# Optimization experiments

Hardware: AMD Instinct MI355X
Metric: run time of the kernel (lower is better)

The kernel has to match this reference:

```python
import jax, jax.numpy as jnp
import numpy as np

N1 = 50000; N2 = 50000; F = 256; HID = 64; H = 8; DH = HID // H; L = 2; E = 800000


def setup_inputs() -> dict:
    key = jax.random.key(0)
    ks = jax.random.split(key, 20)
    f32 = jnp.float32
    rn = lambda k, shape, s=0.1: jax.random.normal(k, shape, dtype=f32) * s
    inp = {}
    inp['x1'] = jax.random.normal(ks[0], (N1, F), dtype=f32)
    inp['x2'] = jax.random.normal(ks[1], (N2, F), dtype=f32)
    # row 0 = source node ids, row 1 = destination node ids
    inp['edge12'] = jax.random.randint(ks[2], (2, E), 0, N2)  # n1 -> n2
    inp['edge21'] = jax.random.randint(ks[3], (2, E), 0, N1)  # n2 -> n1
    inp['w_in'] = rn(ks[4], (2, HID, F))
    inp['b_in'] = rn(ks[5], (2, HID))
    inp['kw'] = rn(ks[6], (L, 2, HID, HID)); inp['kb'] = rn(ks[7], (L, 2, HID))
    inp['qw'] = rn(ks[8], (L, 2, HID, HID)); inp['qb'] = rn(ks[9], (L, 2, HID))
    inp['vw'] = rn(ks[10], (L, 2, HID, HID)); inp['vb'] = rn(ks[11], (L, 2, HID))
    inp['aw'] = rn(ks[12], (L, 2, HID, HID)); inp['ab'] = rn(ks[13], (L, 2, HID))
    inp['skip'] = jax.random.normal(ks[14], (L, 2), dtype=f32)
    inp['a_rel'] = rn(ks[15], (L, 2, H, DH, DH), 0.3)
    inp['m_rel'] = rn(ks[16], (L, 2, H, DH, DH), 0.3)
    inp['p_rel'] = jnp.ones((L, 2, H), dtype=f32)
    return inp


def _segment_softmax(logits, seg, n):
    # logits: [E, H], seg: [E] destination ids
    m = jax.ops.segment_max(logits, seg, num_segments=n)
    e = jnp.exp(logits - m[seg])
    s = jax.ops.segment_sum(e, seg, num_segments=n)
    return e / s[seg]


def reference(x1, x2, edge12, edge21, w_in, b_in, kw, kb, qw, qb, vw, vb, aw, ab,
              skip, a_rel, m_rel, p_rel):
    scale = jnp.asarray(1.0 / np.sqrt(DH), x1.dtype)

    def kqv(h, l, t):
        k = (h @ kw[l, t].T + kb[l, t]).reshape(-1, H, DH)
        q = (h @ qw[l, t].T + qb[l, t]).reshape(-1, H, DH)
        v = (h @ vw[l, t].T + vb[l, t]).reshape(-1, H, DH)
        return k, q, v

    def message(k_src, v_src, q_dst, edge, ar, mr, pr, n_dst):
        kr = jnp.einsum('nhd,hde->nhe', k_src, ar)   # per-node relation projection
        vr = jnp.einsum('nhd,hde->nhe', v_src, mr)
        s, d = edge[0], edge[1]
        logit = jnp.einsum('ehd,ehd->eh', q_dst[d], kr[s]) * pr[None, :] * scale
        alpha = _segment_softmax(logit, d, n_dst)     # [E, H]
        out = jax.ops.segment_sum(alpha[:, :, None] * vr[s], d, num_segments=n_dst)
        return out.reshape(n_dst, HID)

    def update(o, h, l, t):
        o = jax.nn.gelu(o, approximate=False) @ aw[l, t].T + ab[l, t]
        beta = jax.nn.sigmoid(skip[l, t])
        return beta * o + (1.0 - beta) * h

    # per-node-type input Linear + ReLU stem
    h1 = jax.nn.relu(x1 @ w_in[0].T + b_in[0])
    h2 = jax.nn.relu(x2 @ w_in[1].T + b_in[1])

    outs1, outs2 = [], []
    for l in range(L):
        k1, q1, v1 = kqv(h1, l, 0)
        k2, q2, v2 = kqv(h2, l, 1)
        o2 = message(k1, v1, q2, edge12, a_rel[l, 0], m_rel[l, 0], p_rel[l, 0], h2.shape[0])
        o1 = message(k2, v2, q1, edge21, a_rel[l, 1], m_rel[l, 1], p_rel[l, 1], h1.shape[0])
        h1 = update(o1, h1, l, 0)
        h2 = update(o2, h2, l, 1)
        outs1.append(h1)
        outs2.append(h2)

    Em = jnp.concatenate(outs1, axis=1)  # [N1, HID*L]
    Ed = jnp.concatenate(outs2, axis=1)  # [N2, HID*L]
    return Em, Ed
```

## Files before the change

kernel.cpp:

```cpp
#include <hip/hip_runtime.h>
#include <hip/hip_bf16.h>
#include <math.h>

typedef __attribute__((ext_vector_type(8))) short bf16x8;
typedef __attribute__((ext_vector_type(4))) float f32x4;
typedef __attribute__((ext_vector_type(4))) unsigned int u32x4;
typedef __attribute__((ext_vector_type(4))) int i32x4;
typedef unsigned short ushort_t;

#define BUCKET_SHIFT 6
#define BUCKET_CAP   64

__device__ inline short f2b(float f) {
    __hip_bfloat16 h = __float2bfloat16(f);
    return __builtin_bit_cast(short, h);
}
__device__ inline float b2f(unsigned short u) {
    return __builtin_bit_cast(float, (unsigned int)u << 16);
}
__device__ inline float blo(unsigned int w) {
    return __builtin_bit_cast(float, w << 16);
}
__device__ inline float bhi(unsigned int w) {
    return __builtin_bit_cast(float, w & 0xffff0000u);
}

__global__ __launch_bounds__(256) void prep_kernel(
    const float* __restrict__ w_in,
    const float* __restrict__ kw, const float* __restrict__ kb,
    const float* __restrict__ qw, const float* __restrict__ qb,
    const float* __restrict__ vw, const float* __restrict__ vb,
    const float* __restrict__ aw,
    const float* __restrict__ a_rel, const float* __restrict__ m_rel,
    const float* __restrict__ p_rel,
    short* __restrict__ wstem, short* __restrict__ Wcat,
    float* __restrict__ Bcat, short* __restrict__ Awb)
{
    int bid = blockIdx.x, tid = threadIdx.x;
    if (bid >= 4) {
        int t = bid - 4;
        for (int i = tid; i < 16384; i += 256)
            wstem[t * 16384 + i] = f2b(w_in[t * 16384 + i]);
        return;
    }
    int base = bid;
    const float* KW = kw + base * 4096;
    const float* QW = qw + base * 4096;
    const float* VW = vw + base * 4096;
    const float* AR = a_rel + base * 512;
    const float* MR = m_rel + base * 512;
    const float* PR = p_rel + base * 8;
    short* WC = Wcat + base * 12288;
    float* BC = Bcat + base * 192;

    for (int i = tid; i < 4096; i += 256) WC[i] = f2b(QW[i]);
    for (int i = tid; i < 4096; i += 256) {
        int out = i >> 6, in = i & 63;
        int h = out >> 3, e = out & 7;
        float s = PR[h] * 0.35355339059327373f;
        float acc = 0.f;
        #pragma unroll
        for (int d = 0; d < 8; ++d) acc += KW[(h * 8 + d) * 64 + in] * AR[h * 64 + d * 8 + e];
        WC[4096 + i] = f2b(acc * s);
    }
    for (int i = tid; i < 4096; i += 256) {
        int out = i >> 6, in = i & 63;
        int h = out >> 3, e = out & 7;
        float acc = 0.f;
        #pragma unroll
        for (int d = 0; d < 8; ++d) acc += VW[(h * 8 + d) * 64 + in] * MR[h * 64 + d * 8 + e];
        WC[8192 + i] = f2b(acc);
    }
    if (tid < 64) {
        BC[tid] = qb[base * 64 + tid];
    } else if (tid < 128) {
        int out = tid - 64;
        int h = out >> 3, e = out & 7;
        float s = PR[h] * 0.35355339059327373f;
        float acc = 0.f;
        #pragma unroll
        for (int d = 0; d < 8; ++d) acc += kb[base * 64 + h * 8 + d] * AR[h * 64 + d * 8 + e];
        BC[64 + out] = acc * s;
    } else if (tid < 192) {
        int out = tid - 128;
        int h = out >> 3, e = out & 7;
        float acc = 0.f;
        #pragma unroll
        for (int d = 0; d < 8; ++d) acc += vb[base * 64 + h * 8 + d] * MR[h * 64 + d * 8 + e];
        BC[128 + out] = acc;
    }
    for (int i = tid; i < 4096; i += 256) Awb[base * 4096 + i] = f2b(aw[base * 4096 + i]);
}

__global__ __launch_bounds__(256) void stem2_mfma(
    const float* __restrict__ X1, const float* __restrict__ X2,
    const short* __restrict__ Wb, const float* __restrict__ B1, const float* __restrict__ B2,
    short* __restrict__ H1, short* __restrict__ H2, int N1, int N2, int nt1)
{
    const float* X; const short* Wsrc; const float* B; short* Hb; int N; int tb;
    if (blockIdx.x < nt1) { X = X1; Wsrc = Wb;         B = B1; Hb = H1; N = N1; tb = blockIdx.x; }
    else                  { X = X2; Wsrc = Wb + 16384; B = B2; Hb = H2; N = N2; tb = blockIdx.x - nt1; }
    __shared__ short Ws[64 * 256];
    int tid = threadIdx.x;
    #pragma unroll
    for (int k = 0; k < 8; ++k) {
        int u = tid + k * 256;
        int row = u >> 5, c = u & 31;
        u32x4 v = *reinterpret_cast<const u32x4*>(Wsrc + row * 256 + c * 8);
        *reinterpret_cast<u32x4*>(&Ws[row * 256 + ((c ^ (row & 7)) << 3)]) = v;
    }
    __syncthreads();
    int w = tid >> 6, l = tid & 63;
    int g = l >> 4, q = l & 15;
    int row = tb * 64 + w * 16 + q;
    bool rok = row < N;
    f32x4 acc[4] = {};
    const float* xr = X + (size_t)row * 256 + g * 8;
    #pragma unroll
    for (int s = 0; s < 8; ++s) {
        bf16x8 a = {};
        if (rok) {
            float4 x0 = *reinterpret_cast<const float4*>(xr + s * 32);
            float4 x1 = *reinterpret_cast<const float4*>(xr + s * 32 + 4);
            a[0] = f2b(x0.x); a[1] = f2b(x0.y); a[2] = f2b(x0.z); a[3] = f2b(x0.w);
            a[4] = f2b(x1.x); a[5] = f2b(x1.y); a[6] = f2b(x1.z); a[7] = f2b(x1.w);
        }
        #pragma unroll
        for (int n = 0; n < 4; ++n) {
            int br = n * 16 + q;
            int c = s * 4 + g;
            bf16x8 b = *reinterpret_cast<bf16x8*>(&Ws[br * 256 + ((c ^ (br & 7)) << 3)]);
            acc[n] = __builtin_amdgcn_mfma_f32_16x16x32_bf16(a, b, acc[n], 0, 0, 0);
        }
    }
    int orow0 = tb * 64 + w * 16 + g * 4;
    #pragma unroll
    for (int n = 0; n < 4; ++n) {
        int col = n * 16 + q;
        float bias = B[col];
        #pragma unroll
        for (int r = 0; r < 4; ++r) {
            int orow = orow0 + r;
            if (orow < N)
                Hb[(size_t)orow * 64 + col] = f2b(fmaxf(acc[n][r] + bias, 0.f));
        }
    }
}

__global__ __launch_bounds__(256) void kqv2_mfma(
    const short* __restrict__ H1, const short* __restrict__ Wc1, const float* __restrict__ Bc1,
    short* __restrict__ Q1, short* __restrict__ KV1, int N1,
    const short* __restrict__ H2, const short* __restrict__ Wc2, const float* __restrict__ Bc2,
    short* __restrict__ Q2, short* __restrict__ KV2, int N2, int nt1)
{
    const short* Hb; const short* Wcat; const float* Bcat; short* Qb; short* KV; int N; int tb;
    if (blockIdx.x < nt1) { Hb = H1; Wcat = Wc1; Bcat = Bc1; Qb = Q1; KV = KV1; N = N1; tb = blockIdx.x; }
    else                  { Hb = H2; Wcat = Wc2; Bcat = Bc2; Qb = Q2; KV = KV2; N = N2; tb = blockIdx.x - nt1; }
    __shared__ short Ws[192 * 64];
    int tid = threadIdx.x;
    #pragma unroll
    for (int k = 0; k < 6; ++k) {
        int u = tid + k * 256;
        int row = u >> 3, c = u & 7;
        u32x4 v = *reinterpret_cast<const u32x4*>(Wcat + row * 64 + c * 8);
        *reinterpret_cast<u32x4*>(&Ws[row * 64 + ((c ^ (row & 7)) << 3)]) = v;
    }
    __syncthreads();
    int w = tid >> 6, l = tid & 63;
    int g = l >> 4, q = l & 15;
    int arow = tb * 64 + w * 16 + q;
    bool rok = arow < N;
    bf16x8 a0 = {}, a1 = {};
    if (rok) {
        a0 = *reinterpret_cast<const bf16x8*>(Hb + (size_t)arow * 64 + g * 8);
        a1 = *reinterpret_cast<const bf16x8*>(Hb + (size_t)arow * 64 + 32 + g * 8);
    }
    f32x4 acc[12] = {};
    #pragma unroll
    for (int n = 0; n < 12; ++n) {
        int br = n * 16 + q;
        bf16x8 b0 = *reinterpret_cast<bf16x8*>(&Ws[br * 64 + ((0 * 4 + g) ^ (br & 7)) * 8]);
        acc[n] = __builtin_amdgcn_mfma_f32_16x16x32_bf16(a0, b0, acc[n], 0, 0, 0);
        bf16x8 b1 = *reinterpret_cast<bf16x8*>(&Ws[br * 64 + ((1 * 4 + g) ^ (br & 7)) * 8]);
        acc[n] = __builtin_amdgcn_mfma_f32_16x16x32_bf16(a1, b1, acc[n], 0, 0, 0);
    }
    int orow0 = tb * 64 + w * 16 + g * 4;
    #pragma unroll
    for (int n = 0; n < 12; ++n) {
        int col = n * 16 + q;
        float bias = Bcat[col];
        #pragma unroll
        for (int r = 0; r < 4; ++r) {
            int orow = orow0 + r;
            if (orow < N) {
                float v = acc[n][r] + bias;
                if (n < 4)      Qb[(size_t)orow * 64 + col]                 = f2b(v);
                else if (n < 8) KV[(size_t)orow * 128 + 2 * (col - 64)]     = f2b(v);
                else            KV[(size_t)orow * 128 + 2 * (col - 128) + 1] = f2b(v);
            }
        }
    }
}

__global__ __launch_bounds__(256) void bucket8v_kernel(
    const int* __restrict__ srcA, const int* __restrict__ dstA,
    const int* __restrict__ srcB, const int* __restrict__ dstB,
    int* __restrict__ cntA, int* __restrict__ cntB,
    ushort_t* __restrict__ csA, ushort_t* __restrict__ csB,
    int E, int rangeA, int rangeB, int G)
{
    int grp = blockIdx.x & 7;
    int blk = blockIdx.x >> 3;
    int loA = grp * rangeA, hiA = loA + rangeA;
    int loB = grp * rangeB, hiB = loB + rangeB;
    int stride = G * 256;
    int E4 = E >> 2;
    for (int v = blk * 256 + threadIdx.x; v < 2 * E4; v += stride) {
        if (v < E4) {
            i32x4 d4 = __builtin_nontemporal_load(reinterpret_cast<const i32x4*>(dstA) + v);
            int base = v * 4;
            if (d4.x >= loA && d4.x < hiA) { int p = atomicAdd(&cntA[d4.x], 1); if (p < BUCKET_CAP) csA[((size_t)d4.x << BUCKET_SHIFT) + p] = (ushort_t)srcA[base]; }
            if (d4.y >= loA && d4.y < hiA) { int p = atomicAdd(&cntA[d4.y], 1); if (p < BUCKET_CAP) csA[((size_t)d4.y << BUCKET_SHIFT) + p] = (ushort_t)srcA[base + 1]; }
            if (d4.z >= loA && d4.z < hiA) { int p = atomicAdd(&cntA[d4.z], 1); if (p < BUCKET_CAP) csA[((size_t)d4.z << BUCKET_SHIFT) + p] = (ushort_t)srcA[base + 2]; }
            if (d4.w >= loA && d4.w < hiA) { int p = atomicAdd(&cntA[d4.w], 1); if (p < BUCKET_CAP) csA[((size_t)d4.w << BUCKET_SHIFT) + p] = (ushort_t)srcA[base + 3]; }
        } else {
            int vv = v - E4;
            i32x4 d4 = __builtin_nontemporal_load(reinterpret_cast<const i32x4*>(dstB) + vv);
            int base = vv * 4;
            if (d4.x >= loB && d4.x < hiB) { int p = atomicAdd(&cntB[d4.x], 1); if (p < BUCKET_CAP) csB[((size_t)d4.x << BUCKET_SHIFT) + p] = (ushort_t)srcB[base]; }
            if (d4.y >= loB && d4.y < hiB) { int p = atomicAdd(&cntB[d4.y], 1); if (p < BUCKET_CAP) csB[((size_t)d4.y << BUCKET_SHIFT) + p] = (ushort_t)srcB[base + 1]; }
            if (d4.z >= loB && d4.z < hiB) { int p = atomicAdd(&cntB[d4.z], 1); if (p < BUCKET_CAP) csB[((size_t)d4.z << BUCKET_SHIFT) + p] = (ushort_t)srcB[base + 2]; }
            if (d4.w >= loB && d4.w < hiB) { int p = atomicAdd(&cntB[d4.w], 1); if (p < BUCKET_CAP) csB[((size_t)d4.w << BUCKET_SHIFT) + p] = (ushort_t)srcB[base + 3]; }
        }
    }
    int tail = E & 3;
    if (blk == 0 && threadIdx.x < 2 * tail) {
        int t = threadIdx.x;
        if (t < tail) {
            int i = E - tail + t;
            int d = dstA[i];
            if (d >= loA && d < hiA) { int p = atomicAdd(&cntA[d], 1); if (p < BUCKET_CAP) csA[((size_t)d << BUCKET_SHIFT) + p] = (ushort_t)srcA[i]; }
        } else {
            int i = E - tail + (t - tail);
            int d = dstB[i];
            if (d >= loB && d < hiB) { int p = atomicAdd(&cntB[d], 1); if (p < BUCKET_CAP) csB[((size_t)d << BUCKET_SHIFT) + p] = (ushort_t)srcB[i]; }
        }
    }
}

__global__ __launch_bounds__(256) void gather8_kernel(
    const int* __restrict__ cntA, const ushort_t* __restrict__ csA,
    const short* __restrict__ QA, const short* __restrict__ KVA, short* __restrict__ GA, int NA,
    const int* __restrict__ cntB, const ushort_t* __restrict__ csB,
    const short* __restrict__ QB, const short* __restrict__ KVB, short* __restrict__ GB, int NB)
{
    int grp = blockIdx.x & 7;
    int localBlock = (blockIdx.x >> 3) * 4 + (grp & 3);
    const int* cnt; const ushort_t* cs; const short* Qb; const short* KV; short* G; int N;
    if (grp < 4) { cnt = cntA; cs = csA; Qb = QA; KV = KVA; G = GA; N = NA; }
    else         { cnt = cntB; cs = csB; Qb = QB; KV = KVB; G = GB; N = NB; }
    int d = localBlock * 4 + (threadIdx.x >> 6);
    if (d >= N) return;
    int lane = threadIdx.x & 63;
    int j = lane & 15;
    int sub = lane >> 4;
    int deg = min(cnt[d], BUCKET_CAP);
    uint2 qw = *reinterpret_cast<const uint2*>(Qb + (size_t)d * 64 + 4 * j);
    float q0 = blo(qw.x), q1 = bhi(qw.x), q2 = blo(qw.y), q3 = bhi(qw.y);
    float a0 = 0.f, a1 = 0.f, a2 = 0.f, a3 = 0.f, den = 0.f;
    int idv = (lane < deg) ? (int)cs[((size_t)d << BUCKET_SHIFT) + lane] : 0;
    for (int i = 0; i < deg; i += 4) {
        int idx = i + sub;
        bool valid = idx < deg;
        int s = __shfl(idv, valid ? idx : 0);
        u32x4 w = *reinterpret_cast<const u32x4*>(KV + (size_t)s * 128 + 8 * j);
        float t = q0 * blo(w.x);
        t = fmaf(q1, blo(w.y), t);
        t = fmaf(q2, blo(w.z), t);
        t = fmaf(q3, blo(w.w), t);
        t += __shfl_xor(t, 1);
        float e = valid ? __expf(t) : 0.f;
        den += e;
        a0 = fmaf(e, bhi(w.x), a0);
        a1 = fmaf(e, bhi(w.y), a1);
        a2 = fmaf(e, bhi(w.z), a2);
        a3 = fmaf(e, bhi(w.w), a3);
    }
    a0 += __shfl_xor(a0, 16); a1 += __shfl_xor(a1, 16);
    a2 += __shfl_xor(a2, 16); a3 += __shfl_xor(a3, 16);
    den += __shfl_xor(den, 16);
    a0 += __shfl_xor(a0, 32); a1 += __shfl_xor(a1, 32);
    a2 += __shfl_xor(a2, 32); a3 += __shfl_xor(a3, 32);
    den += __shfl_xor(den, 32);
    if (lane < 16) {
        float r = (den > 0.f) ? 1.f / den : 0.f;
        float o0 = a0 * r, o1 = a1 * r, o2 = a2 * r, o3 = a3 * r;
        float g0 = 0.5f * o0 * (1.f + erff(o0 * 0.70710678118654752f));
        float g1 = 0.5f * o1 * (1.f + erff(o1 * 0.70710678118654752f));
        float g2 = 0.5f * o2 * (1.f + erff(o2 * 0.70710678118654752f));
        float g3 = 0.5f * o3 * (1.f + erff(o3 * 0.70710678118654752f));
        uint2 pw;
        pw.x = ((unsigned int)(unsigned short)f2b(g0)) | (((unsigned int)(unsigned short)f2b(g1)) << 16);
        pw.y = ((unsigned int)(unsigned short)f2b(g2)) | (((unsigned int)(unsigned short)f2b(g3)) << 16);
        *reinterpret_cast<uint2*>(G + (size_t)d * 64 + 4 * j) = pw;
    }
}

__global__ __launch_bounds__(256) void updkqv_mfma(
    const short* __restrict__ G1, const short* __restrict__ Aw1, const float* __restrict__ Ab1,
    const float* __restrict__ sk1, short* __restrict__ H1, float* __restrict__ Out1, int N1,
    const short* __restrict__ G2, const short* __restrict__ Aw2, const float* __restrict__ Ab2,
    const float* __restrict__ sk2, short* __restrict__ H2, float* __restrict__ Out2, int N2,
    const short* __restrict__ Wc1n, const float* __restrict__ Bc1n,
    short* __restrict__ Q1, short* __restrict__ KV1,
    const short* __restrict__ Wc2n, const float* __restrict__ Bc2n,
    short* __restrict__ Q2, short* __restrict__ KV2,
    int nt1, int outColOff)
{
    const short* G; const short* Awb; const float* Ab; const float* skipp;
    short* Hb; float* Out; int N; int tb;
    const short* Wcat; const float* Bcat; short* Qb; short* KV;
    if (blockIdx.x < nt1) {
        G = G1; Awb = Aw1; Ab = Ab1; skipp = sk1; Hb = H1; Out = Out1; N = N1; tb = blockIdx.x;
        Wcat = Wc1n; Bcat = Bc1n; Qb = Q1; KV = KV1;
    } else {
        G = G2; Awb = Aw2; Ab = Ab2; skipp = sk2; Hb = H2; Out = Out2; N = N2; tb = blockIdx.x - nt1;
        Wcat = Wc2n; Bcat = Bc2n; Qb = Q2; KV = KV2;
    }
    __shared__ short Ws[192 * 64];
    __shared__ short hs[64][64];
    int tid = threadIdx.x;
    #pragma unroll
    for (int k = 0; k < 6; ++k) {
        int u = tid + k * 256;
        int row = u >> 3, c = u & 7;
        u32x4 v = *reinterpret_cast<const u32x4*>(Wcat + row * 64 + c * 8);
        *reinterpret_cast<u32x4*>(&Ws[row * 64 + ((c ^ (row & 7)) << 3)]) = v;
    }
    int w = tid >> 6, l = tid & 63;
    int g = l >> 4, q = l & 15;
    bf16x8 bfw[4][2];
    #pragma unroll
    for (int n = 0; n < 4; ++n)
        #pragma unroll
        for (int s = 0; s < 2; ++s)
            bfw[n][s] = *reinterpret_cast<const bf16x8*>(Awb + (n * 16 + q) * 64 + s * 32 + g * 8);
    float beta = 1.f / (1.f + __expf(-skipp[0]));
    int arow = tb * 64 + w * 16 + q;
    bool rok = arow < N;
    bf16x8 ua0 = {}, ua1 = {};
    if (rok) {
        ua0 = *reinterpret_cast<const bf16x8*>(G + (size_t)arow * 64 + g * 8);
        ua1 = *reinterpret_cast<const bf16x8*>(G + (size_t)arow * 64 + 32 + g * 8);
    }
    f32x4 uacc[4] = {};
    #pragma unroll
    for (int n = 0; n < 4; ++n) {
        uacc[n] = __builtin_amdgcn_mfma_f32_16x16x32_bf16(ua0, bfw[n][0], uacc[n], 0, 0, 0);
        uacc[n] = __builtin_amdgcn_mfma_f32_16x16x32_bf16(ua1, bfw[n][1], uacc[n], 0, 0, 0);
    }
    int orow0 = tb * 64 + w * 16 + g * 4;
    int lrow0 = w * 16 + g * 4;
    #pragma unroll
    for (int n = 0; n < 4; ++n) {
        int col = n * 16 + q;
        float bias = Ab[col];
        #pragma unroll
        for (int r = 0; r < 4; ++r) {
            int orow = orow0 + r;
            if (orow < N) {
                float hold = b2f(((const unsigned short*)Hb)[(size_t)orow * 64 + col]);
                float hnew = beta * (uacc[n][r] + bias) + (1.f - beta) * hold;
                short hb16 = f2b(hnew);
                Out[(size_t)orow * 128 + outColOff + col] = hnew;
                Hb[(size_t)orow * 64 + col] = hb16;
                hs[lrow0 + r][col] = hb16;
            } else {
                hs[lrow0 + r][col] = 0;
            }
        }
    }
    __syncthreads();
    bf16x8 a0 = *reinterpret_cast<const bf16x8*>(&hs[w * 16 + q][g * 8]);
    bf16x8 a1 = *reinterpret_cast<const bf16x8*>(&hs[w * 16 + q][32 + g * 8]);
    f32x4 acc[12] = {};
    #pragma unroll
    for (int n = 0; n < 12; ++n) {
        int br = n * 16 + q;
        bf16x8 b0 = *reinterpret_cast<bf16x8*>(&Ws[br * 64 + ((0 * 4 + g) ^ (br & 7)) * 8]);
        acc[n] = __builtin_amdgcn_mfma_f32_16x16x32_bf16(a0, b0, acc[n], 0, 0, 0);
        bf16x8 b1 = *reinterpret_cast<bf16x8*>(&Ws[br * 64 + ((1 * 4 + g) ^ (br & 7)) * 8]);
        acc[n] = __builtin_amdgcn_mfma_f32_16x16x32_bf16(a1, b1, acc[n], 0, 0, 0);
    }
    #pragma unroll
    for (int n = 0; n < 12; ++n) {
        int col = n * 16 + q;
        float bias = Bcat[col];
        #pragma unroll
        for (int r = 0; r < 4; ++r) {
            int orow = orow0 + r;
            if (orow < N) {
                float v = acc[n][r] + bias;
                if (n < 4)      Qb[(size_t)orow * 64 + col]                  = f2b(v);
                else if (n < 8) KV[(size_t)orow * 128 + 2 * (col - 64)]      = f2b(v);
                else            KV[(size_t)orow * 128 + 2 * (col - 128) + 1] = f2b(v);
            }
        }
    }
}

__global__ __launch_bounds__(256) void update2_mfma(
    const short* __restrict__ G1, const short* __restrict__ Aw1, const float* __restrict__ Ab1,
    const float* __restrict__ sk1, short* __restrict__ H1, float* __restrict__ Out1, int N1,
    const short* __restrict__ G2, const short* __restrict__ Aw2, const float* __restrict__ Ab2,
    const float* __restrict__ sk2, short* __restrict__ H2, float* __restrict__ Out2, int N2,
    int nt1, int outColOff)
{
    const short* G; const short* Awb; const float* Ab; const float* skipp;
    short* Hb; float* Out; int N; int tb;
    if (blockIdx.x < nt1) { G = G1; Awb = Aw1; Ab = Ab1; skipp = sk1; Hb = H1; Out = Out1; N = N1; tb = blockIdx.x; }
    else                  { G = G2; Awb = Aw2; Ab = Ab2; skipp = sk2; Hb = H2; Out = Out2; N = N2; tb = blockIdx.x - nt1; }
    int tid = threadIdx.x;
    int w = tid >> 6, l = tid & 63;
    int g = l >> 4, q = l & 15;
    bf16x8 bf[4][2];
    #pragma unroll
    for (int n = 0; n < 4; ++n)
        #pragma unroll
        for (int s = 0; s < 2; ++s)
            bf[n][s] = *reinterpret_cast<const bf16x8*>(Awb + (n * 16 + q) * 64 + s * 32 + g * 8);
    float beta = 1.f / (1.f + __expf(-skipp[0]));
    int arow = tb * 64 + w * 16 + q;
    bool rok = arow < N;
    bf16x8 a0 = {}, a1 = {};
    if (rok) {
        a0 = *reinterpret_cast<const bf16x8*>(G + (size_t)arow * 64 + g * 8);
        a1 = *reinterpret_cast<const bf16x8*>(G + (size_t)arow * 64 + 32 + g * 8);
    }
    f32x4 acc[4] = {};
    #pragma unroll
    for (int n = 0; n < 4; ++n) {
        acc[n] = __builtin_amdgcn_mfma_f32_16x16x32_bf16(a0, bf[n][0], acc[n], 0, 0, 0);
        acc[n] = __builtin_amdgcn_mfma_f32_16x16x32_bf16(a1, bf[n][1], acc[n], 0, 0, 0);
    }
    int orow0 = tb * 64 + w * 16 + g * 4;
    #pragma unroll
    for (int n = 0; n < 4; ++n) {
        int col = n * 16 + q;
        float bias = Ab[col];
        #pragma unroll
        for (int r = 0; r < 4; ++r) {
            int orow = orow0 + r;
            if (orow < N) {
                float hold = b2f(((const unsigned short*)Hb)[(size_t)orow * 64 + col]);
                float hnew = beta * (acc[n][r] + bias) + (1.f - beta) * hold;
                Out[(size_t)orow * 128 + outColOff + col] = hnew;
                Hb[(size_t)orow * 64 + col] = f2b(hnew);
            }
        }
    }
}

extern "C" void kernel_launch(void* const* d_in, const int* in_sizes, int n_in,
                              void* d_out, int out_size, void* d_ws, size_t ws_size,
                              hipStream_t stream) {
    const float* x1    = (const float*)d_in[0];
    const float* x2    = (const float*)d_in[1];
    const int*   e12   = (const int*)d_in[2];
    const int*   e21   = (const int*)d_in[3];
    const float* w_in  = (const float*)d_in[4];
    const float* b_in  = (const float*)d_in[5];
    const float* kw    = (const float*)d_in[6];
    const float* kb    = (const float*)d_in[7];
    const float* qw    = (const float*)d_in[8];
    const float* qb    = (const float*)d_in[9];
    const float* vw    = (const float*)d_in[10];
    const float* vb    = (const float*)d_in[11];
    const float* aw    = (const float*)d_in[12];
    const float* ab    = (const float*)d_in[13];
    const float* skip  = (const float*)d_in[14];
    const float* a_rel = (const float*)d_in[15];
    const float* m_rel = (const float*)d_in[16];
    const float* p_rel = (const float*)d_in[17];

    int N1 = in_sizes[0] / 256;
    int N2 = in_sizes[1] / 256;
    int E  = in_sizes[2] / 2;

    float* out = (float*)d_out;

    char* wsp = (char*)d_ws;
    auto alloc = [&](size_t bytes) { void* p = wsp; wsp += (bytes + 255) & ~(size_t)255; return p; };
    short* hb1   = (short*)alloc((size_t)N1 * 64 * 2);
    short* hb2   = (short*)alloc((size_t)N2 * 64 * 2);
    short* qb1   = (short*)alloc((size_t)N1 * 64 * 2);
    short* qb2   = (short*)alloc((size_t)N2 * 64 * 2);
    short* kv1   = (short*)alloc((size_t)N1 * 128 * 2);
    short* kv2   = (short*)alloc((size_t)N2 * 128 * 2);
    short* g1    = (short*)alloc((size_t)N1 * 64 * 2);
    short* g2    = (short*)alloc((size_t)N2 * 64 * 2);
    short* wstem = (short*)alloc(2 * 16384 * 2);
    short* WcatB = (short*)alloc(4 * 12288 * 2);
    float* BcatB = (float*)alloc(4 * 192 * 4);
    short* AwbB  = (short*)alloc(4 * 4096 * 2);
    int* cnts    = (int*)alloc((size_t)(N1 + N2) * 4);
    int* cnt12   = cnts;
    int* cnt21   = cnts + N2;
    ushort_t* csr12 = (ushort_t*)alloc(((size_t)N2 << BUCKET_SHIFT) * 2);
    ushort_t* csr21 = (ushort_t*)alloc(((size_t)N1 << BUCKET_SHIFT) * 2);

    const int BLK = 256;
    int nt1 = (N1 + 63) / 64;
    int nt2 = (N2 + 63) / 64;

    int rangeA = (N2 + 7) / 8;
    int rangeB = (N1 + 7) / 8;
    const int G8 = 512;

    prep_kernel<<<6, BLK, 0, stream>>>(w_in, kw, kb, qw, qb, vw, vb, aw,
                                       a_rel, m_rel, p_rel, wstem, WcatB, BcatB, AwbB);

    hipMemsetAsync(cnts, 0, (size_t)(N1 + N2) * 4, stream);
    bucket8v_kernel<<<8 * G8, BLK, 0, stream>>>(e12, e12 + E, e21, e21 + E,
                                                cnt12, cnt21, csr12, csr21,
                                                E, rangeA, rangeB, G8);

    stem2_mfma<<<nt1 + nt2, BLK, 0, stream>>>(x1, x2, wstem, b_in, b_in + 64,
                                              hb1, hb2, N1, N2, nt1);

    int bA = (N2 + 3) / 4;
    int bB = (N1 + 3) / 4;
    int bmax = bA > bB ? bA : bB;
    int nlb = (bmax + 3) / 4;
    int gblocks = 8 * nlb;

    kqv2_mfma<<<nt1 + nt2, BLK, 0, stream>>>(
        hb1, WcatB + (size_t)0 * 12288, BcatB + (size_t)0 * 192, qb1, kv1, N1,
        hb2, WcatB + (size_t)1 * 12288, BcatB + (size_t)1 * 192, qb2, kv2, N2, nt1);

    gather8_kernel<<<gblocks, BLK, 0, stream>>>(
        cnt12, csr12, qb2, kv1, g2, N2,
        cnt21, csr21, qb1, kv2, g1, N1);

    updkqv_mfma<<<nt1 + nt2, BLK, 0, stream>>>(
        g1, AwbB + (size_t)0 * 4096, ab + (size_t)0 * 64, skip + 0, hb1, out, N1,
        g2, AwbB + (size_t)1 * 4096, ab + (size_t)1 * 64, skip + 1, hb2,
        out + (size_t)N1 * 128, N2,
        WcatB + (size_t)2 * 12288, BcatB + (size_t)2 * 192, qb1, kv1,
        WcatB + (size_t)3 * 12288, BcatB + (size_t)3 * 192, qb2, kv2,
        nt1, 0);

    gather8_kernel<<<gblocks, BLK, 0, stream>>>(
        cnt12, csr12, qb2, kv1, g2, N2,
        cnt21, csr21, qb1, kv2, g1, N1);

    update2_mfma<<<nt1 + nt2, BLK, 0, stream>>>(
        g1, AwbB + (size_t)2 * 4096, ab + (size_t)2 * 64, skip + 2, hb1, out, N1,
        g2, AwbB + (size_t)3 * 4096, ab + (size_t)3 * 64, skip + 3, hb2,
        out + (size_t)N1 * 128, N2, nt1, 64);
}
```

Before: 314.0 us.

## Store K/V in fp8 e4m3 and split edge bucketing by direction

The interleaved K/V per-node buffers are now stored as fp8 e4m3 rather than bf16. This halves the bytes read in the random per-edge gather inside the attention aggregation kernel. The edge bucketing kernel is also restructured so that half of the block groups handle each direction over a quarter of the destination range, instead of every group scanning both edge lists. The fp8 storage reduces accuracy of the attention logits and values, which may threaten tolerance.

```diff
diff --git a/kernel.cpp b/kernel.cpp
--- a/kernel.cpp
+++ b/kernel.cpp
@@ -1,5 +1,6 @@
 #include <hip/hip_runtime.h>
 #include <hip/hip_bf16.h>
+#include <hip/hip_fp8.h>
 #include <math.h>
 
 typedef __attribute__((ext_vector_type(8))) short bf16x8;
@@ -7,6 +8,7 @@
 typedef __attribute__((ext_vector_type(4))) unsigned int u32x4;
 typedef __attribute__((ext_vector_type(4))) int i32x4;
 typedef unsigned short ushort_t;
+typedef unsigned char uchar_t;
 
 #define BUCKET_SHIFT 6
 #define BUCKET_CAP   64
@@ -23,6 +25,15 @@
 }
 __device__ inline float bhi(unsigned int w) {
     return __builtin_bit_cast(float, w & 0xffff0000u);
+}
+__device__ inline uchar_t f2f8(float f) {
+    __hip_fp8_e4m3 h(f);
+    return (uchar_t)h.__x;
+}
+__device__ inline float f82f(unsigned int u) {
+    __hip_fp8_e4m3 h;
+    h.__x = (__hip_fp8_storage_t)(u & 0xff);
+    return (float)h;
 }
 
 __global__ __launch_bounds__(256) void prep_kernel(
@@ -149,11 +160,11 @@
 
 __global__ __launch_bounds__(256) void kqv2_mfma(
     const short* __restrict__ H1, const short* __restrict__ Wc1, const float* __restrict__ Bc1,
-    short* __restrict__ Q1, short* __restrict__ KV1, int N1,
+    short* __restrict__ Q1, uchar_t* __restrict__ KV1, int N1,
     const short* __restrict__ H2, const short* __restrict__ Wc2, const float* __restrict__ Bc2,
-    short* __restrict__ Q2, short* __restrict__ KV2, int N2, int nt1)
-{
-    const short* Hb; const short* Wcat; const float* Bcat; short* Qb; short* KV; int N; int tb;
+    short* __restrict__ Q2, uchar_t* __restrict__ KV2, int N2, int nt1)
+{
+    const short* Hb; const short* Wcat; const float* Bcat; short* Qb; uchar_t* KV; int N; int tb;
     if (blockIdx.x < nt1) { Hb = H1; Wcat = Wc1; Bcat = Bc1; Qb = Q1; KV = KV1; N = N1; tb = blockIdx.x; }
     else                  { Hb = H2; Wcat = Wc2; Bcat = Bc2; Qb = Q2; KV = KV2; N = N2; tb = blockIdx.x - nt1; }
     __shared__ short Ws[192 * 64];
@@ -194,69 +205,58 @@
             int orow = orow0 + r;
             if (orow < N) {
                 float v = acc[n][r] + bias;
-                if (n < 4)      Qb[(size_t)orow * 64 + col]                 = f2b(v);
-                else if (n < 8) KV[(size_t)orow * 128 + 2 * (col - 64)]     = f2b(v);
-                else            KV[(size_t)orow * 128 + 2 * (col - 128) + 1] = f2b(v);
+                if (n < 4)      Qb[(size_t)orow * 64 + col]              = f2b(v);
+                else if (n < 8) KV[(size_t)orow * 128 + 2 * (col - 64)]  = f2f8(v);
+                else            KV[(size_t)orow * 128 + 2 * (col - 128) + 1] = f2f8(v);
             }
         }
     }
 }
 
-__global__ __launch_bounds__(256) void bucket8v_kernel(
-    const int* __restrict__ srcA, const int* __restrict__ dstA,
-    const int* __restrict__ srcB, const int* __restrict__ dstB,
-    int* __restrict__ cntA, int* __restrict__ cntB,
-    ushort_t* __restrict__ csA, ushort_t* __restrict__ csB,
-    int E, int rangeA, int rangeB, int G)
+__global__ __launch_bounds__(256) void bucket8d_kernel(
+    const int* __restrict__ e12, const int* __restrict__ e21,
+    int* __restrict__ cnt12, int* __restrict__ cnt21,
+    ushort_t* __restrict__ cs12, ushort_t* __restrict__ cs21,
+    int E, int N1, int N2, int G)
 {
     int grp = blockIdx.x & 7;
     int blk = blockIdx.x >> 3;
-    int loA = grp * rangeA, hiA = loA + rangeA;
-    int loB = grp * rangeB, hiB = loB + rangeB;
+    bool dirA = grp < 4;
+    const int* srcp = dirA ? e12 : e21;
+    const int* dstp = dirA ? (e12 + E) : (e21 + E);
+    int* cnt = dirA ? cnt12 : cnt21;
+    ushort_t* cs = dirA ? cs12 : cs21;
+    int Nn = dirA ? N2 : N1;
+    int qr = grp & 3;
+    int range = (Nn + 3) >> 2;
+    int lo = qr * range, hi = lo + range;
+    int E4 = E >> 2;
     int stride = G * 256;
-    int E4 = E >> 2;
-    for (int v = blk * 256 + threadIdx.x; v < 2 * E4; v += stride) {
-        if (v < E4) {
-            i32x4 d4 = __builtin_nontemporal_load(reinterpret_cast<const i32x4*>(dstA) + v);
-            int base = v * 4;
-            if (d4.x >= loA && d4.x < hiA) { int p = atomicAdd(&cntA[d4.x], 1); if (p < BUCKET_CAP) csA[((size_t)d4.x << BUCKET_SHIFT) + p] = (ushort_t)srcA[base]; }
-            if (d4.y >= loA && d4.y < hiA) { int p = atomicAdd(&cntA[d4.y], 1); if (p < BUCKET_CAP) csA[((size_t)d4.y << BUCKET_SHIFT) + p] = (ushort_t)srcA[base + 1]; }
-            if (d4.z >= loA && d4.z < hiA) { int p = atomicAdd(&cntA[d4.z], 1); if (p < BUCKET_CAP) csA[((size_t)d4.z << BUCKET_SHIFT) + p] = (ushort_t)srcA[base + 2]; }
-            if (d4.w >= loA && d4.w < hiA) { int p = atomicAdd(&cntA[d4.w], 1); if (p < BUCKET_CAP) csA[((size_t)d4.w << BUCKET_SHIFT) + p] = (ushort_t)srcA[base + 3]; }
-        } else {
-            int vv = v - E4;
-            i32x4 d4 = __builtin_nontemporal_load(reinterpret_cast<const i32x4*>(dstB) + vv);
-            int base = vv * 4;
-            if (d4.x >= loB && d4.x < hiB) { int p = atomicAdd(&cntB[d4.x], 1); if (p < BUCKET_CAP) csB[((size_t)d4.x << BUCKET_SHIFT) + p] = (ushort_t)srcB[base]; }
-            if (d4.y >= loB && d4.y < hiB) { int p = atomicAdd(&cntB[d4.y], 1); if (p < BUCKET_CAP) csB[((size_t)d4.y << BUCKET_SHIFT) + p] = (ushort_t)srcB[base + 1]; }
-            if (d4.z >= loB && d4.z < hiB) { int p = atomicAdd(&cntB[d4.z], 1); if (p < BUCKET_CAP) csB[((size_t)d4.z << BUCKET_SHIFT) + p] = (ushort_t)srcB[base + 2]; }
-            if (d4.w >= loB && d4.w < hiB) { int p = atomicAdd(&cntB[d4.w], 1); if (p < BUCKET_CAP) csB[((size_t)d4.w << BUCKET_SHIFT) + p] = (ushort_t)srcB[base + 3]; }
-        }
+    for (int v = blk * 256 + threadIdx.x; v < E4; v += stride) {
+        i32x4 d4 = __builtin_nontemporal_load(reinterpret_cast<const i32x4*>(dstp) + v);
+        int base = v * 4;
+        if (d4.x >= lo && d4.x < hi) { int p = atomicAdd(&cnt[d4.x], 1); if (p < BUCKET_CAP) cs[((size_t)d4.x << BUCKET_SHIFT) + p] = (ushort_t)srcp[base]; }
+        if (d4.y >= lo && d4.y < hi) { int p = atomicAdd(&cnt[d4.y], 1); if (p < BUCKET_CAP) cs[((size_t)d4.y << BUCKET_SHIFT) + p] = (ushort_t)srcp[base + 1]; }
+        if (d4.z >= lo && d4.z < hi) { int p = atomicAdd(&cnt[d4.z], 1); if (p < BUCKET_CAP) cs[((size_t)d4.z << BUCKET_SHIFT) + p] = (ushort_t)srcp[base + 2]; }
+        if (d4.w >= lo && d4.w < hi) { int p = atomicAdd(&cnt[d4.w], 1); if (p < BUCKET_CAP) cs[((size_t)d4.w << BUCKET_SHIFT) + p] = (ushort_t)srcp[base + 3]; }
     }
     int tail = E & 3;
-    if (blk == 0 && threadIdx.x < 2 * tail) {
-        int t = threadIdx.x;
-        if (t < tail) {
-            int i = E - tail + t;
-            int d = dstA[i];
-            if (d >= loA && d < hiA) { int p = atomicAdd(&cntA[d], 1); if (p < BUCKET_CAP) csA[((size_t)d << BUCKET_SHIFT) + p] = (ushort_t)srcA[i]; }
-        } else {
-            int i = E - tail + (t - tail);
-            int d = dstB[i];
-            if (d >= loB && d < hiB) { int p = atomicAdd(&cntB[d], 1); if (p < BUCKET_CAP) csB[((size_t)d << BUCKET_SHIFT) + p] = (ushort_t)srcB[i]; }
-        }
+    if (blk == 0 && threadIdx.x < tail) {
+        int i = E - tail + threadIdx.x;
+        int d = dstp[i];
+        if (d >= lo && d < hi) { int p = atomicAdd(&cnt[d], 1); if (p < BUCKET_CAP) cs[((size_t)d << BUCKET_SHIFT) + p] = (ushort_t)srcp[i]; }
     }
 }
 
 __global__ __launch_bounds__(256) void gather8_kernel(
     const int* __restrict__ cntA, const ushort_t* __restrict__ csA,
-    const short* __restrict__ QA, const short* __restrict__ KVA, short* __restrict__ GA, int NA,
+    const short* __restrict__ QA, const uchar_t* __restrict__ KVA, short* __restrict__ GA, int NA,
     const int* __restrict__ cntB, const ushort_t* __restrict__ csB,
-    const short* __restrict__ QB, const short* __restrict__ KVB, short* __restrict__ GB, int NB)
+    const short* __restrict__ QB, const uchar_t* __restrict__ KVB, short* __restrict__ GB, int NB)
 {
     int grp = blockIdx.x & 7;
     int localBlock = (blockIdx.x >> 3) * 4 + (grp & 3);
-    const int* cnt; const ushort_t* cs; const short* Qb; const short* KV; short* G; int N;
+    const int* cnt; const ushort_t* cs; const short* Qb; const uchar_t* KV; short* G; int N;
     if (grp < 4) { cnt = cntA; cs = csA; Qb = QA; KV = KVA; G = GA; N = NA; }
     else         { cnt = cntB; cs = csB; Qb = QB; KV = KVB; G = GB; N = NB; }
     int d = localBlock * 4 + (threadIdx.x >> 6);
@@ -273,18 +273,22 @@
         int idx = i + sub;
         bool valid = idx < deg;
         int s = __shfl(idv, valid ? idx : 0);
-        u32x4 w = *reinterpret_cast<const u32x4*>(KV + (size_t)s * 128 + 8 * j);
-        float t = q0 * blo(w.x);
-        t = fmaf(q1, blo(w.y), t);
-        t = fmaf(q2, blo(w.z), t);
-        t = fmaf(q3, blo(w.w), t);
+        uint2 wv = *reinterpret_cast<const uint2*>(KV + (size_t)s * 128 + 8 * j);
+        float k0 = f82f(wv.x),       v0 = f82f(wv.x >> 8);
+        float k1 = f82f(wv.x >> 16), v1 = f82f(wv.x >> 24);
+        float k2 = f82f(wv.y),       v2 = f82f(wv.y >> 8);
+        float k3 = f82f(wv.y >> 16), v3 = f82f(wv.y >> 24);
+        float t = q0 * k0;
+        t = fmaf(q1, k1, t);
+        t = fmaf(q2, k2, t);
+        t = fmaf(q3, k3, t);
         t += __shfl_xor(t, 1);
         float e = valid ? __expf(t) : 0.f;
         den += e;
-        a0 = fmaf(e, bhi(w.x), a0);
-        a1 = fmaf(e, bhi(w.y), a1);
-        a2 = fmaf(e, bhi(w.z), a2);
-        a3 = fmaf(e, bhi(w.w), a3);
+        a0 = fmaf(e, v0, a0);
+        a1 = fmaf(e, v1, a1);
+        a2 = fmaf(e, v2, a2);
+        a3 = fmaf(e, v3, a3);
     }
     a0 += __shfl_xor(a0, 16); a1 += __shfl_xor(a1, 16);
     a2 += __shfl_xor(a2, 16); a3 += __shfl_xor(a3, 16);
@@ -312,14 +316,14 @@
     const short* __restrict__ G2, const short* __restrict__ Aw2, const float* __restrict__ Ab2,
     const float* __restrict__ sk2, short* __restrict__ H2, float* __restrict__ Out2, int N2,
     const short* __restrict__ Wc1n, const float* __restrict__ Bc1n,
-    short* __restrict__ Q1, short* __restrict__ KV1,
+    short* __restrict__ Q1, uchar_t* __restrict__ KV1,
     const short* __restrict__ Wc2n, const float* __restrict__ Bc2n,
-    short* __restrict__ Q2, short* __restrict__ KV2,
+    short* __restrict__ Q2, uchar_t* __restrict__ KV2,
     int nt1, int outColOff)
 {
     const short* G; const short* Awb; const float* Ab; const float* skipp;
     short* Hb; float* Out; int N; int tb;
-    const short* Wcat; const float* Bcat; short* Qb; short* KV;
+    const short* Wcat; const float* Bcat; short* Qb; uchar_t* KV;
     if (blockIdx.x < nt1) {
         G = G1; Awb = Aw1; Ab = Ab1; skipp = sk1; Hb = H1; Out = Out1; N = N1; tb = blockIdx.x;
         Wcat = Wc1n; Bcat = Bc1n; Qb = Q1; KV = KV1;
@@ -401,9 +405,9 @@
             int orow = orow0 + r;
             if (orow < N) {
                 float v = acc[n][r] + bias;
-                if (n < 4)      Qb[(size_t)orow * 64 + col]                  = f2b(v);
-                else if (n < 8) KV[(size_t)orow * 128 + 2 * (col - 64)]      = f2b(v);
-                else            KV[(size_t)orow * 128 + 2 * (col - 128) + 1] = f2b(v);
+                if (n < 4)      Qb[(size_t)orow * 64 + col]              = f2b(v);
+                else if (n < 8) KV[(size_t)orow * 128 + 2 * (col - 64)]  = f2f8(v);
+                else            KV[(size_t)orow * 128 + 2 * (col - 128) + 1] = f2f8(v);
             }
         }
     }
@@ -495,8 +499,8 @@
     short* hb2   = (short*)alloc((size_t)N2 * 64 * 2);
     short* qb1   = (short*)alloc((size_t)N1 * 64 * 2);
     short* qb2   = (short*)alloc((size_t)N2 * 64 * 2);
-    short* kv1   = (short*)alloc((size_t)N1 * 128 * 2);
-    short* kv2   = (short*)alloc((size_t)N2 * 128 * 2);
+    uchar_t* kv1 = (uchar_t*)alloc((size_t)N1 * 128);
+    uchar_t* kv2 = (uchar_t*)alloc((size_t)N2 * 128);
     short* g1    = (short*)alloc((size_t)N1 * 64 * 2);
     short* g2    = (short*)alloc((size_t)N2 * 64 * 2);
     short* wstem = (short*)alloc(2 * 16384 * 2);
@@ -512,18 +516,14 @@
     const int BLK = 256;
     int nt1 = (N1 + 63) / 64;
     int nt2 = (N2 + 63) / 64;
-
-    int rangeA = (N2 + 7) / 8;
-    int rangeB = (N1 + 7) / 8;
     const int G8 = 512;
 
     prep_kernel<<<6, BLK, 0, stream>>>(w_in, kw, kb, qw, qb, vw, vb, aw,
                                        a_rel, m_rel, p_rel, wstem, WcatB, BcatB, AwbB);
 
     hipMemsetAsync(cnts, 0, (size_t)(N1 + N2) * 4, stream);
-    bucket8v_kernel<<<8 * G8, BLK, 0, stream>>>(e12, e12 + E, e21, e21 + E,
-                                                cnt12, cnt21, csr12, csr21,
-                                                E, rangeA, rangeB, G8);
+    bucket8d_kernel<<<8 * G8, BLK, 0, stream>>>(e12, e21, cnt12, cnt21,
+                                                csr12, csr21, E, N1, N2, G8);
 
     stem2_mfma<<<nt1 + nt2, BLK, 0, stream>>>(x1, x2, wstem, b_in, b_in + 64,
                                               hb1, hb2, N1, N2, nt1);
```

Measured after the change: 302.0 us. 3.8% less time.
